# Performance work log

Hardware: AMD Instinct MI355X
Metric: run time of the kernel (lower is better)

## Reference

```python
import jax, jax.numpy as jnp
import numpy as np

DIM = 128
GROUPS = [1, 2, 2, 3]


def setup_inputs() -> dict:
    key = jax.random.key(0)
    ks = jax.random.split(key, 8)
    c = DIM
    def p(k, shape, scale=0.02):
        return jax.random.normal(k, shape, dtype=jnp.float32) * scale
    return {
        "x": jax.random.normal(ks[0], (8, c, 128, 128), dtype=jnp.float32),
        "temperature": jnp.ones((4, 1, 1), dtype=jnp.float32),
        "w_qkv": p(ks[1], (3 * c, c)),            # Conv2d(dim, 3*dim, 1), bias=False
        "w_dw": p(ks[2], (3 * c, 1, 3, 3)),        # depthwise 3x3, groups=3*dim
        "w_proj": p(ks[3], (c, c)),                # Conv2d(dim, dim, 1), bias=False
        "w_gate": p(ks[4], (c, c)),                # Intra gatingConv (Conv1d k=1)
        "b_gate": jnp.zeros((c,), jnp.float32),
        "w_down": p(ks[5], (c // 2, c)),           # Intra down
        "b_down": jnp.zeros((c // 2,), jnp.float32),
        "w_up": p(ks[6], (c, c // 2)),             # Intra up
        "b_up": jnp.zeros((c,), jnp.float32),
    }


def _group_sizes(c):
    total = sum(GROUPS)
    sizes = [int(r / total * c) for r in GROUPS]
    sizes[-1] += c - sum(sizes)
    return sizes


def _forward(x, temperature, w_qkv, w_dw, w_proj, w_gate, b_gate,
             w_down, b_down, w_up, b_up):
    b, c, h, w = x.shape
    L = h * w
    # qkv = dwconv3x3(conv1x1(x))
    qkv = jnp.einsum('bchw,oc->bohw', x, w_qkv)
    qkv = jax.lax.conv_general_dilated(
        qkv, w_dw, (1, 1), 'SAME', feature_group_count=3 * c,
        dimension_numbers=('NCHW', 'OIHW', 'NCHW'))
    q, k, v = jnp.split(qkv.reshape(b, 3 * c, L), 3, axis=1)
    # ReGroup: sort channels by mean q activation (descending), split into groups
    channel_mean = q.mean(axis=(0, 2))            # (c,)
    idx = jnp.argsort(-channel_mean)
    q, k, v = q[:, idx], k[:, idx], v[:, idx]
    sizes = _group_sizes(c)
    outs, caches, cache_means = [], [], []
    start = 0
    for i, g in enumerate(sizes):
        qg = q[:, start:start + g]
        kg = k[:, start:start + g]
        vg = v[:, start:start + g]
        start += g
        qn = qg / jnp.maximum(jnp.linalg.norm(qg, axis=-1, keepdims=True), 1e-12)
        kn = kg / jnp.maximum(jnp.linalg.norm(kg, axis=-1, keepdims=True), 1e-12)
        attn = jax.nn.softmax(
            jnp.einsum('bcl,bdl->bcd', qn, kn) * temperature[i, 0, 0], axis=-1)
        outs.append(jnp.einsum('bcd,bdl->bcl', attn, vg))   # (b, g, L)
        tc = jax.lax.stop_gradient(qn + kn)                 # detached cache
        caches.append(tc)
        # per-group mean over L, channel-tiled/padded to c (for cache update)
        gm = tc.mean(axis=-1)                               # (b, g)
        rep = max(1, c // g)
        gm = jnp.tile(gm, (1, rep))
        gm = gm[:, :c] if gm.shape[1] >= c else jnp.pad(gm, ((0, 0), (0, c - gm.shape[1])))
        cache_means.append(gm)
    out_all = jnp.concatenate(outs, axis=1)       # (b, c, L)
    tmp_caches = jnp.concatenate(caches, axis=1)  # (b, c, L)
    # CalculateCurrentLayerCache: bilinear upsample of (1,1) map == broadcast
    s = int(L ** 0.5 + 0.9999)
    acc = sum(cache_means) / float(len(cache_means))        # (b, c)
    qv_cache = jnp.broadcast_to((acc * 0.9)[:, :, None, None], (b, c, s, s))
    # Intra cache modulation: gated = gelu(conv(x1+x2)) * (x1+x2); up(down(gated))
    sxy = out_all + tmp_caches
    gating = jax.nn.gelu(jnp.einsum('bcl,oc->bol', sxy, w_gate) + b_gate[:, None],
                         approximate=False)
    gated = gating * sxy
    mod = jnp.einsum('bcl,oc->bol', gated, w_down) + b_down[:, None]
    mod = jnp.einsum('bcl,oc->bol', mod, w_up) + b_up[:, None]
    out_all = mod + out_all
    out_all = jnp.einsum('bchw,oc->bohw', out_all.reshape(b, c, h, w), w_proj)
    return out_all, qv_cache


def reference(x, temperature, w_qkv, w_dw, w_proj, w_gate, b_gate,
              w_down, b_down, w_up, b_up):
    return _forward(x, temperature, w_qkv, w_dw, w_proj, w_gate, b_gate,
                    w_down, b_down, w_up, b_up)
```

## Files before the change

kernel.cpp:

```cpp
#include <hip/hip_runtime.h>
#include <math.h>

#define B_ 8
#define C_ 128
#define O3_ 384
#define H_ 128
#define W_ 128
#define L_ 16384
#define NS_ 64
#define MAXP_ 2304

typedef float f32x4 __attribute__((ext_vector_type(4)));
typedef short bf16x8 __attribute__((ext_vector_type(8)));

static __device__ __forceinline__ ushort f2bf(float f) {
    uint u = __float_as_uint(f);
    u += 0x7fffu + ((u >> 16) & 1u);
    return (ushort)(u >> 16);
}
static __device__ __forceinline__ float bf2f(ushort h) {
    return __uint_as_float(((uint)h) << 16);
}

__global__ __launch_bounds__(256) void transp_k(const float* __restrict__ x,
    short* __restrict__ xhi, short* __restrict__ xlo)
{
    __shared__ float t[128][33];
    const int b = blockIdx.y;
    const int l0 = blockIdx.x * 32;
    const int tid = threadIdx.x;
    {
        const int c = tid >> 1, half = tid & 1;
        const float* src = x + ((size_t)b * C_ + c) * L_ + l0 + half * 16;
#pragma unroll
        for (int u = 0; u < 4; u++) {
            float4 v = *reinterpret_cast<const float4*>(src + u * 4);
            t[c][half * 16 + u * 4 + 0] = v.x;
            t[c][half * 16 + u * 4 + 1] = v.y;
            t[c][half * 16 + u * 4 + 2] = v.z;
            t[c][half * 16 + u * 4 + 3] = v.w;
        }
    }
    __syncthreads();
    {
        const int l = tid >> 3, strip = tid & 7;
        uint hi[8], lo[8];
#pragma unroll
        for (int i = 0; i < 8; i++) {
            float a0 = t[strip * 16 + 2 * i][l], a1 = t[strip * 16 + 2 * i + 1][l];
            ushort h0 = f2bf(a0), h1 = f2bf(a1);
            ushort g0 = f2bf(a0 - bf2f(h0)), g1 = f2bf(a1 - bf2f(h1));
            hi[i] = (uint)h0 | ((uint)h1 << 16);
            lo[i] = (uint)g0 | ((uint)g1 << 16);
        }
        size_t ob = ((size_t)b * L_ + l0 + l) * C_ + strip * 16;
        uint4* ph = reinterpret_cast<uint4*>(xhi + ob);
        uint4* pl = reinterpret_cast<uint4*>(xlo + ob);
        ph[0] = *reinterpret_cast<uint4*>(&hi[0]);
        ph[1] = *reinterpret_cast<uint4*>(&hi[4]);
        pl[0] = *reinterpret_cast<uint4*>(&lo[0]);
        pl[1] = *reinterpret_cast<uint4*>(&lo[4]);
    }
}

template<int KD, int OT, int MODE>
__global__ __launch_bounds__(256) void mgemm_k(
    const float* __restrict__ Wf, const float* __restrict__ bias,
    const short* __restrict__ Ahi, const short* __restrict__ Alo,
    const float* __restrict__ E0,
    float* __restrict__ Yf, short* __restrict__ Yhi, short* __restrict__ Ylo)
{
    constexpr int NR = OT / 32;
    __shared__ short sAh[128][40];
    __shared__ short sAl[128][40];
    __shared__ short sBh[OT][40];
    __shared__ short sBl[OT][40];
    const int tid = threadIdx.x;
    const int lane = tid & 63;
    const int wid = tid >> 6;
    const int wr = wid >> 1, wc = wid & 1;
    const int oB = blockIdx.x * OT;
    const int lB = blockIdx.y * 128;
    const int ON = gridDim.x * OT;
    const int b = blockIdx.z;
    const int ln15 = lane & 15, lg = lane >> 4;

    f32x4 acc[4][NR];
#pragma unroll
    for (int m = 0; m < 4; m++)
#pragma unroll
        for (int n = 0; n < NR; n++)
#pragma unroll
            for (int r = 0; r < 4; r++) acc[m][n][r] = 0.f;

    for (int kc = 0; kc < KD; kc += 32) {
        for (int p = tid; p < 512; p += 256) {
            int l = p >> 2, c8 = (p & 3) * 8;
            size_t g = ((size_t)b * L_ + lB + l) * KD + kc + c8;
            *reinterpret_cast<bf16x8*>(&sAh[l][c8]) = *reinterpret_cast<const bf16x8*>(&Ahi[g]);
            *reinterpret_cast<bf16x8*>(&sAl[l][c8]) = *reinterpret_cast<const bf16x8*>(&Alo[g]);
        }
        for (int p = tid; p < OT * 8; p += 256) {
            int o = p >> 3, c4 = (p & 7) * 4;
            float4 v = *reinterpret_cast<const float4*>(&Wf[(size_t)(oB + o) * KD + kc + c4]);
            ushort h0 = f2bf(v.x), h1 = f2bf(v.y), h2 = f2bf(v.z), h3 = f2bf(v.w);
            ushort g0 = f2bf(v.x - bf2f(h0)), g1 = f2bf(v.y - bf2f(h1));
            ushort g2 = f2bf(v.z - bf2f(h2)), g3 = f2bf(v.w - bf2f(h3));
            uint2 uh = {(uint)h0 | ((uint)h1 << 16), (uint)h2 | ((uint)h3 << 16)};
            uint2 ul = {(uint)g0 | ((uint)g1 << 16), (uint)g2 | ((uint)g3 << 16)};
            *reinterpret_cast<uint2*>(&sBh[o][c4]) = uh;
            *reinterpret_cast<uint2*>(&sBl[o][c4]) = ul;
        }
        __syncthreads();
        bf16x8 Ah[4], Al[4];
#pragma unroll
        for (int m = 0; m < 4; m++) {
            int row = wr * 64 + m * 16 + ln15;
            Ah[m] = *reinterpret_cast<const bf16x8*>(&sAh[row][lg * 8]);
            Al[m] = *reinterpret_cast<const bf16x8*>(&sAl[row][lg * 8]);
        }
#pragma unroll
        for (int n = 0; n < NR; n++) {
            int brow = wc * (OT / 2) + n * 16 + ln15;
            bf16x8 Bh = *reinterpret_cast<const bf16x8*>(&sBh[brow][lg * 8]);
            bf16x8 Bl = *reinterpret_cast<const bf16x8*>(&sBl[brow][lg * 8]);
#pragma unroll
            for (int m = 0; m < 4; m++) {
                acc[m][n] = __builtin_amdgcn_mfma_f32_16x16x32_bf16(Ah[m], Bh, acc[m][n], 0, 0, 0);
                acc[m][n] = __builtin_amdgcn_mfma_f32_16x16x32_bf16(Ah[m], Bl, acc[m][n], 0, 0, 0);
                acc[m][n] = __builtin_amdgcn_mfma_f32_16x16x32_bf16(Al[m], Bh, acc[m][n], 0, 0, 0);
            }
        }
        __syncthreads();
    }

#pragma unroll
    for (int m = 0; m < 4; m++) {
        const int lg4 = lB + wr * 64 + m * 16 + lg * 4;
#pragma unroll
        for (int n = 0; n < NR; n++) {
            const int o = oB + wc * (OT / 2) + n * 16 + ln15;
            if constexpr (MODE == 4) {
                float4 r4 = {acc[m][n][0], acc[m][n][1], acc[m][n][2], acc[m][n][3]};
                *reinterpret_cast<float4*>(&Yf[((size_t)b * ON + o) * L_ + lg4]) = r4;
            } else {
                float bv = bias[o];
#pragma unroll
                for (int r = 0; r < 4; r++) {
                    size_t yi = ((size_t)b * L_ + lg4 + r) * ON + o;
                    float a = acc[m][n][r] + bv;
                    if constexpr (MODE == 1) {
                        float sxy = bf2f((ushort)Ahi[yi]) + bf2f((ushort)Alo[yi]);
                        a = 0.5f * a * (1.f + erff(a * 0.70710678118654752f)) * sxy;
                    }
                    if constexpr (MODE == 3) a += E0[yi];
                    ushort h = f2bf(a);
                    ushort g = f2bf(a - bf2f(h));
                    Yhi[yi] = (short)h;
                    Ylo[yi] = (short)g;
                }
            }
        }
    }
}

__global__ __launch_bounds__(256) void dwconv_k(const float* __restrict__ in,
    const float* __restrict__ wdw, float* __restrict__ outp,
    float* __restrict__ sumq, float* __restrict__ sumk,
    float* __restrict__ ssq, float* __restrict__ ssk)
{
    const int ch = blockIdx.x, b = blockIdx.y;
    const int tid = threadIdx.x;
    const int tx = tid & 31, band = tid >> 5;
    const int x0 = tx * 4;
    const int y0 = band * 16;
    const size_t base = ((size_t)b * O3_ + ch) * L_;
    const float* wp = wdw + ch * 9;
    float w0 = wp[0], w1 = wp[1], w2 = wp[2], w3 = wp[3], w4 = wp[4],
          w5 = wp[5], w6 = wp[6], w7 = wp[7], w8 = wp[8];

    float s1 = 0.f, s2 = 0.f;
    float b0[6], b1[6], b2[6];

    auto loadrow = [&](int gy, float* r) {
        if ((unsigned)gy < (unsigned)H_) {
            const float* rp = in + base + (size_t)gy * W_;
            float4 m = *reinterpret_cast<const float4*>(rp + x0);
            r[0] = (x0 > 0) ? rp[x0 - 1] : 0.f;
            r[1] = m.x; r[2] = m.y; r[3] = m.z; r[4] = m.w;
            r[5] = (x0 < W_ - 4) ? rp[x0 + 4] : 0.f;
        } else {
            r[0] = r[1] = r[2] = r[3] = r[4] = r[5] = 0.f;
        }
    };
    auto conv3 = [&](const float* ra, const float* rb, const float* rc, int yy) {
        float o0 = ra[0]*w0 + ra[1]*w1 + ra[2]*w2 + rb[0]*w3 + rb[1]*w4 + rb[2]*w5 + rc[0]*w6 + rc[1]*w7 + rc[2]*w8;
        float o1 = ra[1]*w0 + ra[2]*w1 + ra[3]*w2 + rb[1]*w3 + rb[2]*w4 + rb[3]*w5 + rc[1]*w6 + rc[2]*w7 + rc[3]*w8;
        float o2 = ra[2]*w0 + ra[3]*w1 + ra[4]*w2 + rb[2]*w3 + rb[3]*w4 + rb[4]*w5 + rc[2]*w6 + rc[3]*w7 + rc[4]*w8;
        float o3 = ra[3]*w0 + ra[4]*w1 + ra[5]*w2 + rb[3]*w3 + rb[4]*w4 + rb[5]*w5 + rc[3]*w6 + rc[4]*w7 + rc[5]*w8;
        float4 o4 = {o0, o1, o2, o3};
        *reinterpret_cast<float4*>(&outp[base + (size_t)(y0 + yy) * W_ + x0]) = o4;
        s1 += (o0 + o1) + (o2 + o3);
        s2 += o0*o0 + o1*o1 + o2*o2 + o3*o3;
    };

    loadrow(y0 - 1, b0);
    loadrow(y0,     b1);
#pragma unroll
    for (int y3 = 0; y3 < 15; y3 += 3) {
        loadrow(y0 + y3 + 1, b2); conv3(b0, b1, b2, y3);
        loadrow(y0 + y3 + 2, b0); conv3(b1, b2, b0, y3 + 1);
        loadrow(y0 + y3 + 3, b1); conv3(b2, b0, b1, y3 + 2);
    }
    loadrow(y0 + 16, b2); conv3(b0, b1, b2, 15);

    __shared__ float r1[256], r2[256];
    if (ch < 256) {
        r1[tid] = s1; r2[tid] = s2;
        __syncthreads();
        for (int st = 128; st > 0; st >>= 1) {
            if (tid < st) { r1[tid] += r1[tid + st]; r2[tid] += r2[tid + st]; }
            __syncthreads();
        }
        if (tid == 0) {
            if (ch < 128) { sumq[b * 128 + ch] = r1[0]; ssq[b * 128 + ch] = r2[0]; }
            else          { sumk[b * 128 + ch - 128] = r1[0]; ssk[b * 128 + ch - 128] = r2[0]; }
        }
    }
}

__global__ void combine_k(const float* __restrict__ sumq, const float* __restrict__ sumk,
    const float* __restrict__ ssq, const float* __restrict__ ssk,
    int* __restrict__ idxp, float* __restrict__ rqc, float* __restrict__ rkc,
    float* __restrict__ gm)
{
    const int t = threadIdx.x;
    __shared__ double cms[128];
    double s = 0.0;
    for (int b = 0; b < B_; b++) s += (double)sumq[b * 128 + t];
    cms[t] = s;
    float rqv[B_], rkv[B_];
    for (int b = 0; b < B_; b++) {
        rqv[b] = 1.f / fmaxf(sqrtf(ssq[b * 128 + t]), 1e-12f);
        rkv[b] = 1.f / fmaxf(sqrtf(ssk[b * 128 + t]), 1e-12f);
        rqc[b * 128 + t] = rqv[b];
        rkc[b * 128 + t] = rkv[b];
    }
    __syncthreads();
    const double mv = cms[t];
    int r = 0;
    for (int j = 0; j < 128; j++) {
        double o = cms[j];
        if (o > mv || (o == mv && j < t)) r++;
    }
    idxp[r] = t;
    for (int b = 0; b < B_; b++)
        gm[b * 128 + r] = (rqv[b] * sumq[b * 128 + t] + rkv[b] * sumk[b * 128 + t]) * (1.0f / L_);
}

template<int G>
__global__ __launch_bounds__(256) void score_k(const float* __restrict__ dw, const int* __restrict__ idxp,
    int start, int gi, float* __restrict__ spart)
{
    constexpr int TS = G / 16;
    const int split = blockIdx.x, b = blockIdx.y;
    const int tid = threadIdx.x, tx = tid & 15, ty = tid >> 4;
    __shared__ float sQ[G][66];
    __shared__ float sK[G][66];
    __shared__ int sc[G];
    if (tid < G) sc[tid] = idxp[start + tid];
    __syncthreads();

    float acc[TS][TS];
#pragma unroll
    for (int i = 0; i < TS; i++)
#pragma unroll
        for (int j = 0; j < TS; j++) acc[i][j] = 0.f;

    const int l0 = split * (L_ / NS_);
    constexpr int LPT = (G * 64) / 256;
    for (int chk = 0; chk < L_ / NS_; chk += 64) {
#pragma unroll
        for (int i = 0; i < LPT; i++) {
            int id = tid + i * 256;
            int row = id >> 6, lc = id & 63;
            size_t base = ((size_t)b * O3_ + sc[row]) * L_ + l0 + chk + lc;
            sQ[row][lc] = dw[base];
            sK[row][lc] = dw[base + (size_t)128 * L_];
        }
        __syncthreads();
#pragma unroll
        for (int kk = 0; kk < 64; kk++) {
            float qv[TS], kv[TS];
#pragma unroll
            for (int j = 0; j < TS; j++) { qv[j] = sQ[ty * TS + j][kk]; kv[j] = sK[tx * TS + j][kk]; }
#pragma unroll
            for (int i = 0; i < TS; i++)
#pragma unroll
                for (int j = 0; j < TS; j++)
                    acc[i][j] = fmaf(qv[i], kv[j], acc[i][j]);
        }
        __syncthreads();
    }
    float* op = spart + (((size_t)(b * 4 + gi)) * NS_ + split) * MAXP_;
#pragma unroll
    for (int i = 0; i < TS; i++)
#pragma unroll
        for (int j = 0; j < TS; j++)
            op[(ty * TS + i) * G + tx * TS + j] = acc[i][j];
}

__global__ __launch_bounds__(256) void softmax_k(const float* __restrict__ spart,
    const float* __restrict__ rqc, const float* __restrict__ rkc, const int* __restrict__ idxp,
    const float* __restrict__ temp, float* __restrict__ attn)
{
    const int gi = blockIdx.x, b = blockIdx.y;
    const int g = (gi == 0) ? 16 : (gi == 3 ? 48 : 32);
    const int start = (gi == 0) ? 0 : (gi == 1 ? 16 : (gi == 2 ? 48 : 80));
    __shared__ float S[MAXP_];
    __shared__ int sidx[48];
    if (threadIdx.x < g) sidx[threadIdx.x] = idxp[start + threadIdx.x];
    __syncthreads();
    const float tv = temp[gi];
    for (int p = threadIdx.x; p < g * g; p += 256) {
        float s = 0.f;
        const float* sp = spart + ((size_t)(b * 4 + gi)) * NS_ * MAXP_ + p;
        for (int k = 0; k < NS_; k++) s += sp[(size_t)k * MAXP_];
        int cc = p / g, dd = p - cc * g;
        S[p] = s * rqc[b * 128 + sidx[cc]] * rkc[b * 128 + sidx[dd]] * tv;
    }
    __syncthreads();
    const int wv = threadIdx.x >> 6, lane = threadIdx.x & 63;
    for (int r = wv; r < g; r += 4) {
        float val = (lane < g) ? S[r * g + lane] : -1e30f;
        float mx = val;
        for (int m = 32; m > 0; m >>= 1) mx = fmaxf(mx, __shfl_xor(mx, m));
        float e = (lane < g) ? expf(val - mx) : 0.f;
        float sum = e;
        for (int m = 32; m > 0; m >>= 1) sum += __shfl_xor(sum, m);
        if (lane < g) attn[((size_t)(b * 4 + gi)) * MAXP_ + r * g + lane] = e / sum;
    }
}

template<int G>
__global__ __launch_bounds__(256) void av3_k(const float* __restrict__ dw, const int* __restrict__ idxp,
    const float* __restrict__ rqc, const float* __restrict__ rkc,
    const float* __restrict__ attn, int start, int gi,
    float* __restrict__ outallT, short* __restrict__ sxyhi, short* __restrict__ sxylo)
{
    constexpr int C4 = G / 4;
    constexpr int GP = G + 1;
    const int b = blockIdx.y;
    const int lB = blockIdx.x * 64;
    const int tid = threadIdx.x;
    __shared__ float sA[G * GP];
    __shared__ float sV[64][GP];
    __shared__ int cv[G];
    __shared__ float rqs[G], rks[G];
    if (tid < G) {
        int c0 = idxp[start + tid];
        cv[tid] = c0;
        rqs[tid] = rqc[b * 128 + c0];
        rks[tid] = rkc[b * 128 + c0];
    }
    for (int p = tid; p < G * G; p += 256) {
        int cc = p / G, dd = p - cc * G;
        sA[cc * GP + dd] = attn[((size_t)(b * 4 + gi)) * MAXP_ + p];
    }
    __syncthreads();
    for (int idx = tid; idx < 64 * G; idx += 256) {
        int l = idx & 63, d = idx >> 6;
        sV[l][d] = dw[((size_t)b * O3_ + 256 + cv[d]) * L_ + lB + l];
    }
    __syncthreads();
    const int strip = tid & 3, l = tid >> 2;
    float acc[C4];
#pragma unroll
    for (int j = 0; j < C4; j++) acc[j] = 0.f;
    for (int d = 0; d < G; d++) {
        float vd = sV[l][d];
#pragma unroll
        for (int j = 0; j < C4; j++)
            acc[j] = fmaf(sA[(strip * C4 + j) * GP + d], vd, acc[j]);
    }
    const size_t ob = ((size_t)b * L_ + lB + l) * C_ + start + strip * C4;
    float sv[C4];
#pragma unroll
    for (int j = 0; j < C4; j++) {
        int c = strip * C4 + j;
        float q = dw[((size_t)b * O3_ + cv[c]) * L_ + lB + l];
        float k = dw[((size_t)b * O3_ + 128 + cv[c]) * L_ + lB + l];
        sv[j] = acc[j] + rqs[c] * q + rks[c] * k;
    }
#pragma unroll
    for (int j = 0; j < C4; j += 4) {
        float4 o4 = {acc[j], acc[j + 1], acc[j + 2], acc[j + 3]};
        *reinterpret_cast<float4*>(&outallT[ob + j]) = o4;
    }
#pragma unroll
    for (int j = 0; j < C4; j += 2) {
        ushort h0 = f2bf(sv[j]), h1 = f2bf(sv[j + 1]);
        ushort g0 = f2bf(sv[j] - bf2f(h0)), g1 = f2bf(sv[j + 1] - bf2f(h1));
        *reinterpret_cast<uint*>(&sxyhi[ob + j]) = (uint)h0 | ((uint)h1 << 16);
        *reinterpret_cast<uint*>(&sxylo[ob + j]) = (uint)g0 | ((uint)g1 << 16);
    }
}

__global__ __launch_bounds__(256) void qvc_k(const float* __restrict__ gm, float* __restrict__ outq)
{
    const int cpos = blockIdx.x, b = blockIdx.y;
    const float* g = gm + b * 128;
    float v = g[cpos & 15] + g[16 + (cpos & 31)] + g[48 + (cpos & 31)];
    if (cpos < 96) v += g[80 + (cpos % 48)];
    v *= 0.225f;
    float4 vv = {v, v, v, v};
    float4* op = reinterpret_cast<float4*>(outq + ((size_t)b * C_ + cpos) * L_);
    for (int i = threadIdx.x; i < L_ / 4; i += 256) op[i] = vv;
}

extern "C" void kernel_launch(void* const* d_in, const int* in_sizes, int n_in,
                              void* d_out, int out_size, void* d_ws, size_t ws_size,
                              hipStream_t stream)
{
    const float* x     = (const float*)d_in[0];
    const float* temp  = (const float*)d_in[1];
    const float* wqkv  = (const float*)d_in[2];
    const float* wdw   = (const float*)d_in[3];
    const float* wproj = (const float*)d_in[4];
    const float* wgate = (const float*)d_in[5];
    const float* bgate = (const float*)d_in[6];
    const float* wdown = (const float*)d_in[7];
    const float* bdown = (const float*)d_in[8];
    const float* wup   = (const float*)d_in[9];
    const float* bup   = (const float*)d_in[10];
    float* out = (float*)d_out;
    float* ws  = (float*)d_ws;

    float* qkvCL = ws;
    float* dwCL  = ws + 50331648ull;
    short* xThi  = (short*)(ws + 50331648ull);
    short* xTlo  = xThi + 16777216ull;
    float* outallT = ws;
    short* sxyhi   = (short*)(ws + 16777216ull);
    short* sxylo   = sxyhi + 16777216ull;
    short* gatedhi = (short*)(ws + 33554432ull);
    short* gatedlo = gatedhi + 16777216ull;
    short* mod1hi  = (short*)(ws + 16777216ull);
    short* mod1lo  = mod1hi + 8388608ull;
    short* out2hi  = (short*)(ws + 33554432ull);
    short* out2lo  = out2hi + 16777216ull;

    float* spart = out;
    float* attn  = out + 4718592ull;
    float* sumq  = out + 4800000ull;
    float* sumk  = out + 4801024ull;
    float* ssq   = out + 4802048ull;
    float* ssk   = out + 4803072ull;
    float* rqc   = out + 4804096ull;
    float* rkc   = out + 4805120ull;
    float* gm    = out + 4806144ull;
    int*   idxp  = (int*)(out + 4807168ull);

    transp_k<<<dim3(512, 8), 256, 0, stream>>>(x, xThi, xTlo);
    mgemm_k<128, 128, 4><<<dim3(3, 128, 8), 256, 0, stream>>>(
        wqkv, nullptr, xThi, xTlo, nullptr, qkvCL, nullptr, nullptr);
    dwconv_k<<<dim3(384, 8), 256, 0, stream>>>(qkvCL, wdw, dwCL, sumq, sumk, ssq, ssk);
    combine_k<<<1, 128, 0, stream>>>(sumq, sumk, ssq, ssk, idxp, rqc, rkc, gm);
    score_k<16><<<dim3(NS_, 8), 256, 0, stream>>>(dwCL, idxp, 0, 0, spart);
    score_k<32><<<dim3(NS_, 8), 256, 0, stream>>>(dwCL, idxp, 16, 1, spart);
    score_k<32><<<dim3(NS_, 8), 256, 0, stream>>>(dwCL, idxp, 48, 2, spart);
    score_k<48><<<dim3(NS_, 8), 256, 0, stream>>>(dwCL, idxp, 80, 3, spart);
    softmax_k<<<dim3(4, 8), 256, 0, stream>>>(spart, rqc, rkc, idxp, temp, attn);
    av3_k<16><<<dim3(256, 8), 256, 0, stream>>>(dwCL, idxp, rqc, rkc, attn, 0, 0, outallT, sxyhi, sxylo);
    av3_k<32><<<dim3(256, 8), 256, 0, stream>>>(dwCL, idxp, rqc, rkc, attn, 16, 1, outallT, sxyhi, sxylo);
    av3_k<32><<<dim3(256, 8), 256, 0, stream>>>(dwCL, idxp, rqc, rkc, attn, 48, 2, outallT, sxyhi, sxylo);
    av3_k<48><<<dim3(256, 8), 256, 0, stream>>>(dwCL, idxp, rqc, rkc, attn, 80, 3, outallT, sxyhi, sxylo);
    mgemm_k<128, 128, 1><<<dim3(1, 128, 8), 256, 0, stream>>>(
        wgate, bgate, sxyhi, sxylo, nullptr, nullptr, gatedhi, gatedlo);
    qvc_k<<<dim3(128, 8), 256, 0, stream>>>(gm, out + 16777216ull);
    mgemm_k<128, 64, 2><<<dim3(1, 128, 8), 256, 0, stream>>>(
        wdown, bdown, gatedhi, gatedlo, nullptr, nullptr, mod1hi, mod1lo);
    mgemm_k<64, 128, 3><<<dim3(1, 128, 8), 256, 0, stream>>>(
        wup, bup, mod1hi, mod1lo, outallT, nullptr, out2hi, out2lo);
    mgemm_k<128, 128, 4><<<dim3(1, 128, 8), 256, 0, stream>>>(
        wproj, nullptr, out2hi, out2lo, nullptr, out, nullptr, nullptr);
}
```

Baseline: 828.5 us.

## Pre-split weights to bf16 hi/lo and register-prefetch next K tile in GEMM

Weights are split into bf16 hi/lo pairs once by small dedicated kernels, so the GEMM blocks no longer repeat the float-to-bf16 split for every tile. The GEMM main loop now loads the next K-chunk of A and B into registers while the MFMAs run on the current chunk, then stores them to shared memory after a barrier. This hides global load latency behind compute. In exchange it adds two extra launches, more register pressure, and an extra barrier per iteration. The split weights are kept in spare regions of the output and workspace buffers.

Result: faster. 729.6 us (-11.9%).

```diff
diff --git a/kernel.cpp b/kernel.cpp
--- a/kernel.cpp
+++ b/kernel.cpp
@@ -22,6 +22,40 @@
     return __uint_as_float(((uint)h) << 16);
 }
 
+__global__ __launch_bounds__(256) void wsplit_k(
+    const float* __restrict__ wa, const float* __restrict__ wb,
+    const float* __restrict__ wc, const float* __restrict__ wd,
+    short* __restrict__ ha, short* __restrict__ la,
+    short* __restrict__ hb, short* __restrict__ lb,
+    short* __restrict__ hc, short* __restrict__ lc,
+    short* __restrict__ hd, short* __restrict__ ld)
+{
+    const int sel = blockIdx.y;
+    const float* w = sel == 0 ? wa : (sel == 1 ? wb : (sel == 2 ? wc : wd));
+    short* ph = sel == 0 ? ha : (sel == 1 ? hb : (sel == 2 ? hc : hd));
+    short* pl = sel == 0 ? la : (sel == 1 ? lb : (sel == 2 ? lc : ld));
+    const int n = sel == 0 ? 49152 : (sel == 1 ? 16384 : 8192);
+    const int i = blockIdx.x * 256 + threadIdx.x;
+    if (i < n) {
+        float v = w[i];
+        ushort h = f2bf(v);
+        ph[i] = (short)h;
+        pl[i] = (short)f2bf(v - bf2f(h));
+    }
+}
+
+__global__ __launch_bounds__(256) void wsplit1_k(const float* __restrict__ w,
+    short* __restrict__ ph, short* __restrict__ pl, int n)
+{
+    const int i = blockIdx.x * 256 + threadIdx.x;
+    if (i < n) {
+        float v = w[i];
+        ushort h = f2bf(v);
+        ph[i] = (short)h;
+        pl[i] = (short)f2bf(v - bf2f(h));
+    }
+}
+
 __global__ __launch_bounds__(256) void transp_k(const float* __restrict__ x,
     short* __restrict__ xhi, short* __restrict__ xlo)
 {
@@ -65,12 +99,15 @@
 
 template<int KD, int OT, int MODE>
 __global__ __launch_bounds__(256) void mgemm_k(
-    const float* __restrict__ Wf, const float* __restrict__ bias,
+    const short* __restrict__ Whi, const short* __restrict__ Wlo,
+    const float* __restrict__ bias,
     const short* __restrict__ Ahi, const short* __restrict__ Alo,
     const float* __restrict__ E0,
     float* __restrict__ Yf, short* __restrict__ Yhi, short* __restrict__ Ylo)
 {
     constexpr int NR = OT / 32;
+    constexpr int T = KD / 32;
+    constexpr int BPT = (OT * 4) / 256;
     __shared__ short sAh[128][40];
     __shared__ short sAl[128][40];
     __shared__ short sBh[OT][40];
@@ -85,6 +122,9 @@
     const int b = blockIdx.z;
     const int ln15 = lane & 15, lg = lane >> 4;
 
+    const int al0 = tid >> 2, ac8 = (tid & 3) * 8;
+    const size_t abase = ((size_t)b * L_ + lB + al0) * KD + ac8;
+
     f32x4 acc[4][NR];
 #pragma unroll
     for (int m = 0; m < 4; m++)
@@ -93,25 +133,47 @@
 #pragma unroll
             for (int r = 0; r < 4; r++) acc[m][n][r] = 0.f;
 
-    for (int kc = 0; kc < KD; kc += 32) {
-        for (int p = tid; p < 512; p += 256) {
-            int l = p >> 2, c8 = (p & 3) * 8;
-            size_t g = ((size_t)b * L_ + lB + l) * KD + kc + c8;
-            *reinterpret_cast<bf16x8*>(&sAh[l][c8]) = *reinterpret_cast<const bf16x8*>(&Ahi[g]);
-            *reinterpret_cast<bf16x8*>(&sAl[l][c8]) = *reinterpret_cast<const bf16x8*>(&Alo[g]);
-        }
-        for (int p = tid; p < OT * 8; p += 256) {
-            int o = p >> 3, c4 = (p & 7) * 4;
-            float4 v = *reinterpret_cast<const float4*>(&Wf[(size_t)(oB + o) * KD + kc + c4]);
-            ushort h0 = f2bf(v.x), h1 = f2bf(v.y), h2 = f2bf(v.z), h3 = f2bf(v.w);
-            ushort g0 = f2bf(v.x - bf2f(h0)), g1 = f2bf(v.y - bf2f(h1));
-            ushort g2 = f2bf(v.z - bf2f(h2)), g3 = f2bf(v.w - bf2f(h3));
-            uint2 uh = {(uint)h0 | ((uint)h1 << 16), (uint)h2 | ((uint)h3 << 16)};
-            uint2 ul = {(uint)g0 | ((uint)g1 << 16), (uint)g2 | ((uint)g3 << 16)};
-            *reinterpret_cast<uint2*>(&sBh[o][c4]) = uh;
-            *reinterpret_cast<uint2*>(&sBl[o][c4]) = ul;
-        }
-        __syncthreads();
+    bf16x8 pAh[2], pAl[2], pBh[BPT], pBl[BPT];
+
+    auto ldA = [&](int t) {
+#pragma unroll
+        for (int p = 0; p < 2; p++) {
+            size_t g = abase + (size_t)p * 64 * KD + t * 32;
+            pAh[p] = *reinterpret_cast<const bf16x8*>(Ahi + g);
+            pAl[p] = *reinterpret_cast<const bf16x8*>(Alo + g);
+        }
+    };
+    auto ldB = [&](int t) {
+#pragma unroll
+        for (int p = 0; p < BPT; p++) {
+            int idx = tid + p * 256;
+            int o = idx >> 2, c8 = (idx & 3) * 8;
+            size_t g = (size_t)(oB + o) * KD + t * 32 + c8;
+            pBh[p] = *reinterpret_cast<const bf16x8*>(Whi + g);
+            pBl[p] = *reinterpret_cast<const bf16x8*>(Wlo + g);
+        }
+    };
+    auto stAB = [&]() {
+#pragma unroll
+        for (int p = 0; p < 2; p++) {
+            *reinterpret_cast<bf16x8*>(&sAh[al0 + p * 64][ac8]) = pAh[p];
+            *reinterpret_cast<bf16x8*>(&sAl[al0 + p * 64][ac8]) = pAl[p];
+        }
+#pragma unroll
+        for (int p = 0; p < BPT; p++) {
+            int idx = tid + p * 256;
+            int o = idx >> 2, c8 = (idx & 3) * 8;
+            *reinterpret_cast<bf16x8*>(&sBh[o][c8]) = pBh[p];
+            *reinterpret_cast<bf16x8*>(&sBl[o][c8]) = pBl[p];
+        }
+    };
+
+    ldA(0); ldB(0);
+    stAB();
+    __syncthreads();
+
+    for (int t = 0; t < T; t++) {
+        if (t + 1 < T) { ldA(t + 1); ldB(t + 1); }
         bf16x8 Ah[4], Al[4];
 #pragma unroll
         for (int m = 0; m < 4; m++) {
@@ -132,6 +194,7 @@
             }
         }
         __syncthreads();
+        if (t + 1 < T) { stAB(); __syncthreads(); }
     }
 
 #pragma unroll
@@ -449,6 +512,8 @@
     short* mod1lo  = mod1hi + 8388608ull;
     short* out2hi  = (short*)(ws + 33554432ull);
     short* out2lo  = out2hi + 16777216ull;
+    short* wprojh  = (short*)(ws + 25165824ull);
+    short* wprojl  = wprojh + 16384ull;
 
     float* spart = out;
     float* attn  = out + 4718592ull;
@@ -460,10 +525,20 @@
     float* rkc   = out + 4805120ull;
     float* gm    = out + 4806144ull;
     int*   idxp  = (int*)(out + 4807168ull);
-
+    short* wqkvh = (short*)(out + 4900000ull);
+    short* wqkvl = (short*)(out + 4924576ull);
+    short* wgateh= (short*)(out + 4949152ull);
+    short* wgatel= (short*)(out + 4957344ull);
+    short* wdownh= (short*)(out + 4965536ull);
+    short* wdownl= (short*)(out + 4969632ull);
+    short* wuph  = (short*)(out + 4973728ull);
+    short* wupl  = (short*)(out + 4977824ull);
+
+    wsplit_k<<<dim3(192, 4), 256, 0, stream>>>(wqkv, wgate, wdown, wup,
+        wqkvh, wqkvl, wgateh, wgatel, wdownh, wdownl, wuph, wupl);
     transp_k<<<dim3(512, 8), 256, 0, stream>>>(x, xThi, xTlo);
     mgemm_k<128, 128, 4><<<dim3(3, 128, 8), 256, 0, stream>>>(
-        wqkv, nullptr, xThi, xTlo, nullptr, qkvCL, nullptr, nullptr);
+        wqkvh, wqkvl, nullptr, xThi, xTlo, nullptr, qkvCL, nullptr, nullptr);
     dwconv_k<<<dim3(384, 8), 256, 0, stream>>>(qkvCL, wdw, dwCL, sumq, sumk, ssq, ssk);
     combine_k<<<1, 128, 0, stream>>>(sumq, sumk, ssq, ssk, idxp, rqc, rkc, gm);
     score_k<16><<<dim3(NS_, 8), 256, 0, stream>>>(dwCL, idxp, 0, 0, spart);
@@ -476,12 +551,13 @@
     av3_k<32><<<dim3(256, 8), 256, 0, stream>>>(dwCL, idxp, rqc, rkc, attn, 48, 2, outallT, sxyhi, sxylo);
     av3_k<48><<<dim3(256, 8), 256, 0, stream>>>(dwCL, idxp, rqc, rkc, attn, 80, 3, outallT, sxyhi, sxylo);
     mgemm_k<128, 128, 1><<<dim3(1, 128, 8), 256, 0, stream>>>(
-        wgate, bgate, sxyhi, sxylo, nullptr, nullptr, gatedhi, gatedlo);
+        wgateh, wgatel, bgate, sxyhi, sxylo, nullptr, nullptr, gatedhi, gatedlo);
     qvc_k<<<dim3(128, 8), 256, 0, stream>>>(gm, out + 16777216ull);
     mgemm_k<128, 64, 2><<<dim3(1, 128, 8), 256, 0, stream>>>(
-        wdown, bdown, gatedhi, gatedlo, nullptr, nullptr, mod1hi, mod1lo);
+        wdownh, wdownl, bdown, gatedhi, gatedlo, nullptr, nullptr, mod1hi, mod1lo);
     mgemm_k<64, 128, 3><<<dim3(1, 128, 8), 256, 0, stream>>>(
-        wup, bup, mod1hi, mod1lo, outallT, nullptr, out2hi, out2lo);
+        wuph, wupl, bup, mod1hi, mod1lo, outallT, nullptr, out2hi, out2lo);
+    wsplit1_k<<<64, 256, 0, stream>>>(wproj, wprojh, wprojl, 16384);
     mgemm_k<128, 128, 4><<<dim3(1, 128, 8), 256, 0, stream>>>(
-        wproj, nullptr, out2hi, out2lo, nullptr, out, nullptr, nullptr);
-}
+        wprojh, wprojl, nullptr, out2hi, out2lo, nullptr, out, nullptr, nullptr);
+}
```
